# Performance work log

Hardware: AMD Instinct MI355X
Metric: run time of the kernel (lower is better)

Reference implementation:

```python
import jax, jax.numpy as jnp
import numpy as np

H = 128        # hidden_size
L = 3          # n_layers
VOCAB = 256    # input_size == output_size


def setup_inputs() -> dict:
    key = jax.random.key(0)
    ks = jax.random.split(key, 10)
    s = 1.0 / np.sqrt(H)  # PyTorch LSTM/Linear init scale
    return {
        "x": jax.random.randint(ks[0], (1,), 0, VOCAB),
        "h0": jax.random.normal(ks[1], (L, 1, H), dtype=jnp.float32),
        "c0": jax.random.normal(ks[2], (L, 1, H), dtype=jnp.float32),
        # params
        "emb": jax.random.normal(ks[3], (VOCAB, H), dtype=jnp.float32),
        "w_ih": jax.random.uniform(ks[4], (L, 4 * H, H), minval=-s, maxval=s, dtype=jnp.float32),
        "w_hh": jax.random.uniform(ks[5], (L, 4 * H, H), minval=-s, maxval=s, dtype=jnp.float32),
        "b_ih": jax.random.uniform(ks[6], (L, 4 * H), minval=-s, maxval=s, dtype=jnp.float32),
        "b_hh": jax.random.uniform(ks[7], (L, 4 * H), minval=-s, maxval=s, dtype=jnp.float32),
        "Wd": jax.random.uniform(ks[8], (VOCAB, H), minval=-s, maxval=s, dtype=jnp.float32),
        "bd": jax.random.uniform(ks[9], (VOCAB,), minval=-s, maxval=s, dtype=jnp.float32),
    }


def _lstm_step(inp, h0, c0, w_ih, w_hh, b_ih, b_hh):
    """Single time-step, 3-layer LSTM. inp: [1,H]; h0,c0: [L,1,H]. Dropout in eval mode (identity)."""
    hs, cs = [], []
    h_in = inp
    for l in range(L):
        # PyTorch gate order: input, forget, cell(g), output
        gates = h_in @ w_ih[l].T + h0[l] @ w_hh[l].T + b_ih[l] + b_hh[l]  # [1, 4H]
        i, f, g, o = jnp.split(gates, 4, axis=-1)
        c = jax.nn.sigmoid(f) * c0[l] + jax.nn.sigmoid(i) * jnp.tanh(g)
        h = jax.nn.sigmoid(o) * jnp.tanh(c)
        hs.append(h)
        cs.append(c)
        h_in = h  # inter-layer dropout (p=0.5) is identity in eval mode
    return h_in, jnp.stack(hs), jnp.stack(cs)


def reference(x, h0, c0, emb, w_ih, w_hh, b_ih, b_hh, Wd, bd):
    inp = emb[x].reshape(1, H)                      # encoder: [1, H]
    out, hn, cn = _lstm_step(inp, h0, c0, w_ih, w_hh, b_ih, b_hh)
    # self.dropout(p=0.1) identity in eval mode
    logits = out @ Wd.T + bd                        # decoder: [1, VOCAB]
    return logits, hn, cn
```

## Files before the change

### kernel.cpp

```cpp
#include <hip/hip_runtime.h>
#include <math.h>

#define H 128
#define NL 3
#define VOCAB 256
#define NBL 8
#define NLB (NL*NBL)
#define ND 2
#define NB_TOT (NLB+ND)

#define K_TAG(l) (0x51C0DE00u + (unsigned)(l))

typedef unsigned long long u64;

__device__ __forceinline__ float sigmoidf_(float x) {
    return 1.0f / (1.0f + __expf(-x));
}
__device__ __forceinline__ float fast_tanhf(float x) {
    const float e = __expf(2.0f * x);
    return 1.0f - 2.0f * __frcp_rn(e + 1.0f);
}

__global__ __launch_bounds__(256) void fused_lstm_kernel(
    const int*   __restrict__ x_idx,
    const float* __restrict__ h0,
    const float* __restrict__ c0,
    const float* __restrict__ emb,
    const float* __restrict__ w_ih,
    const float* __restrict__ w_hh,
    const float* __restrict__ b_ih,
    const float* __restrict__ b_hh,
    const float* __restrict__ Wd,
    const float* __restrict__ bd,
    float* __restrict__ logits,
    float* __restrict__ hn,
    float* __restrict__ cn,
    u64*   __restrict__ slots)
{
    __shared__ float s_in[H];
    __shared__ float s_h[H];

    const int t   = threadIdx.x;
    const int bid = blockIdx.x;

    if (bid < NLB) {
        const int l  = bid >> 3;
        const int gb = bid & 7;

        const int ul    = t >> 4;
        const int g     = (t >> 2) & 3;
        const int chunk = t & 3;
        const int unit  = gb * 16 + ul;
        const int grow  = g * H + unit;

        const size_t base = ((size_t)l * 4 * H + grow) * H + chunk * 32;
        const float4* pi = (const float4*)(w_ih + base);
        const float4* ph = (const float4*)(w_hh + base);
        float4 wih[8], whh[8];
#pragma unroll
        for (int i = 0; i < 8; ++i) { wih[i] = pi[i]; whh[i] = ph[i]; }
        float bias = 0.0f;
        if (chunk == 0) bias = b_ih[(size_t)l * 4 * H + grow]
                             + b_hh[(size_t)l * 4 * H + grow];
        float c0reg = 0.0f;
        if ((t & 15) == 0) c0reg = c0[l * H + unit];

        if (t >= 128) {
            const int tl = t - 128;
            s_h[tl] = h0[l * H + tl];
            if (l == 0) s_in[tl] = emb[(size_t)x_idx[0] * H + tl];
        }
        __syncthreads();

        const float4* sh = (const float4*)s_h + chunk * 8;
        float r = bias;
#pragma unroll
        for (int i = 0; i < 8; ++i) {
            float4 a = whh[i], v = sh[i];
            r = fmaf(a.x, v.x, r);  r = fmaf(a.y, v.y, r);
            r = fmaf(a.z, v.z, r);  r = fmaf(a.w, v.w, r);
        }

        if (l > 0) {
            if (t < H) {
                const unsigned want = K_TAG(l - 1);
                u64 v;
                do {
                    v = __hip_atomic_load(&slots[(l - 1) * H + t],
                                          __ATOMIC_RELAXED,
                                          __HIP_MEMORY_SCOPE_AGENT);
                } while ((unsigned)(v >> 32) != want);
                s_in[t] = __uint_as_float((unsigned)v);
            }
        }
        __syncthreads();

        const float4* si = (const float4*)s_in + chunk * 8;
        float acc = r;
#pragma unroll
        for (int i = 0; i < 8; ++i) {
            float4 a = wih[i], v = si[i];
            acc = fmaf(a.x, v.x, acc);  acc = fmaf(a.y, v.y, acc);
            acc = fmaf(a.z, v.z, acc);  acc = fmaf(a.w, v.w, acc);
        }
        acc += __shfl_xor(acc, 1);
        acc += __shfl_xor(acc, 2);
        const int bl = (t & 63) & 48;
        const float iv = __shfl(acc, bl,      64);
        const float fv = __shfl(acc, bl + 4,  64);
        const float gv = __shfl(acc, bl + 8,  64);
        const float ov = __shfl(acc, bl + 12, 64);
        if ((t & 15) == 0) {
            const float c = sigmoidf_(fv) * c0reg + sigmoidf_(iv) * fast_tanhf(gv);
            const float h = sigmoidf_(ov) * fast_tanhf(c);
            cn[l * H + unit] = c;
            hn[l * H + unit] = h;
            const u64 w = ((u64)K_TAG(l) << 32) | (u64)__float_as_uint(h);
            __hip_atomic_store(&slots[l * H + unit], w,
                               __ATOMIC_RELAXED, __HIP_MEMORY_SCOPE_AGENT);
        }
    } else {
        const int db        = bid - NLB;
        const int row_local = t >> 1;
        const int chunk     = t & 1;
        const int drow      = db * 128 + row_local;

        const float4* pw = (const float4*)(Wd + (size_t)drow * H + chunk * 64);
        float4 wd[16];
#pragma unroll
        for (int i = 0; i < 16; ++i) wd[i] = pw[i];
        const float bias = bd[drow];
        asm volatile("" ::: "memory");

        if (t < H) {
            const unsigned want = K_TAG(2);
            u64 v;
            do {
                v = __hip_atomic_load(&slots[2 * H + t],
                                      __ATOMIC_RELAXED,
                                      __HIP_MEMORY_SCOPE_AGENT);
            } while ((unsigned)(v >> 32) != want);
            s_in[t] = __uint_as_float((unsigned)v);
        }
        __syncthreads();

        const float4* sh = (const float4*)s_in + chunk * 16;
        float acc = 0.0f;
#pragma unroll
        for (int i = 0; i < 16; ++i) {
            float4 a = wd[i], v = sh[i];
            acc = fmaf(a.x, v.x, acc); acc = fmaf(a.y, v.y, acc);
            acc = fmaf(a.z, v.z, acc); acc = fmaf(a.w, v.w, acc);
        }
        acc += __shfl_xor(acc, 1);
        if (chunk == 0) logits[drow] = acc + bias;
    }
}

extern "C" void kernel_launch(void* const* d_in, const int* in_sizes, int n_in,
                              void* d_out, int out_size, void* d_ws, size_t ws_size,
                              hipStream_t stream) {
    const int*   x    = (const int*)  d_in[0];
    const float* h0   = (const float*)d_in[1];
    const float* c0   = (const float*)d_in[2];
    const float* emb  = (const float*)d_in[3];
    const float* w_ih = (const float*)d_in[4];
    const float* w_hh = (const float*)d_in[5];
    const float* b_ih = (const float*)d_in[6];
    const float* b_hh = (const float*)d_in[7];
    const float* Wd   = (const float*)d_in[8];
    const float* bd   = (const float*)d_in[9];

    float* out    = (float*)d_out;
    float* logits = out;
    float* hn     = out + VOCAB;
    float* cn     = hn + NL * H;

    u64* slots = (u64*)d_ws;

    fused_lstm_kernel<<<NB_TOT, 256, 0, stream>>>(
        x, h0, c0, emb, w_ih, w_hh, b_ih, b_hh, Wd, bd,
        logits, hn, cn, slots);
}
```

Before: 10.82 us.

## Double LSTM blocks per layer, load h0 into registers, gather gates via shared memory

Splits each layer across 16 blocks of 8 hidden units instead of 8 blocks of 16, halving the per-thread weight slice to 16 elements per matrix and spreading the weight loads over more CUs. h0 is read straight into registers, which removes the shared-memory staging and the first block barrier. Gate values are now collected through a small shared array plus an extra barrier instead of cross-lane shuffles. This trades more blocks spinning on the inter-layer flags, and one added barrier, for lower per-block load latency.

```diff
diff --git a/kernel.cpp b/kernel.cpp
--- a/kernel.cpp
+++ b/kernel.cpp
@@ -4,7 +4,7 @@
 #define H 128
 #define NL 3
 #define VOCAB 256
-#define NBL 8
+#define NBL 16
 #define NLB (NL*NBL)
 #define ND 2
 #define NB_TOT (NLB+ND)
@@ -38,45 +38,40 @@
     u64*   __restrict__ slots)
 {
     __shared__ float s_in[H];
-    __shared__ float s_h[H];
+    __shared__ float s_gates[4][8];
 
     const int t   = threadIdx.x;
     const int bid = blockIdx.x;
 
     if (bid < NLB) {
-        const int l  = bid >> 3;
-        const int gb = bid & 7;
+        const int l  = bid >> 4;
+        const int gb = bid & 15;
 
-        const int ul    = t >> 4;
-        const int g     = (t >> 2) & 3;
-        const int chunk = t & 3;
-        const int unit  = gb * 16 + ul;
-        const int grow  = g * H + unit;
+        const int row_local = t >> 3;
+        const int chunk     = t & 7;
+        const int g    = row_local >> 3;
+        const int jr   = row_local & 7;
+        const int unit = gb * 8 + jr;
+        const int grow = g * H + unit;
 
-        const size_t base = ((size_t)l * 4 * H + grow) * H + chunk * 32;
+        const size_t base = ((size_t)l * 4 * H + grow) * H + chunk * 16;
         const float4* pi = (const float4*)(w_ih + base);
         const float4* ph = (const float4*)(w_hh + base);
-        float4 wih[8], whh[8];
+        const float4* p0 = (const float4*)(h0 + l * H + chunk * 16);
+        float4 wih[4], whh[4], h0v[4];
 #pragma unroll
-        for (int i = 0; i < 8; ++i) { wih[i] = pi[i]; whh[i] = ph[i]; }
+        for (int i = 0; i < 4; ++i) { wih[i] = pi[i]; whh[i] = ph[i]; h0v[i] = p0[i]; }
         float bias = 0.0f;
         if (chunk == 0) bias = b_ih[(size_t)l * 4 * H + grow]
                              + b_hh[(size_t)l * 4 * H + grow];
         float c0reg = 0.0f;
-        if ((t & 15) == 0) c0reg = c0[l * H + unit];
+        if (t < 8) c0reg = c0[l * H + gb * 8 + t];
+        if (l == 0 && t < H) s_in[t] = emb[(size_t)x_idx[0] * H + t];
 
-        if (t >= 128) {
-            const int tl = t - 128;
-            s_h[tl] = h0[l * H + tl];
-            if (l == 0) s_in[tl] = emb[(size_t)x_idx[0] * H + tl];
-        }
-        __syncthreads();
-
-        const float4* sh = (const float4*)s_h + chunk * 8;
         float r = bias;
 #pragma unroll
-        for (int i = 0; i < 8; ++i) {
-            float4 a = whh[i], v = sh[i];
+        for (int i = 0; i < 4; ++i) {
+            float4 a = whh[i], v = h0v[i];
             r = fmaf(a.x, v.x, r);  r = fmaf(a.y, v.y, r);
             r = fmaf(a.z, v.z, r);  r = fmaf(a.w, v.w, r);
         }
@@ -95,28 +90,32 @@
         }
         __syncthreads();
 
-        const float4* si = (const float4*)s_in + chunk * 8;
+        const float4* si = (const float4*)s_in + chunk * 4;
         float acc = r;
 #pragma unroll
-        for (int i = 0; i < 8; ++i) {
+        for (int i = 0; i < 4; ++i) {
             float4 a = wih[i], v = si[i];
             acc = fmaf(a.x, v.x, acc);  acc = fmaf(a.y, v.y, acc);
             acc = fmaf(a.z, v.z, acc);  acc = fmaf(a.w, v.w, acc);
         }
         acc += __shfl_xor(acc, 1);
         acc += __shfl_xor(acc, 2);
-        const int bl = (t & 63) & 48;
-        const float iv = __shfl(acc, bl,      64);
-        const float fv = __shfl(acc, bl + 4,  64);
-        const float gv = __shfl(acc, bl + 8,  64);
-        const float ov = __shfl(acc, bl + 12, 64);
-        if ((t & 15) == 0) {
+        acc += __shfl_xor(acc, 4);
+        if (chunk == 0) s_gates[g][jr] = acc;
+        __syncthreads();
+
+        if (t < 8) {
+            const int u = gb * 8 + t;
+            const float iv = s_gates[0][t];
+            const float fv = s_gates[1][t];
+            const float gv = s_gates[2][t];
+            const float ov = s_gates[3][t];
             const float c = sigmoidf_(fv) * c0reg + sigmoidf_(iv) * fast_tanhf(gv);
             const float h = sigmoidf_(ov) * fast_tanhf(c);
-            cn[l * H + unit] = c;
-            hn[l * H + unit] = h;
+            cn[l * H + u] = c;
+            hn[l * H + u] = h;
             const u64 w = ((u64)K_TAG(l) << 32) | (u64)__float_as_uint(h);
-            __hip_atomic_store(&slots[l * H + unit], w,
+            __hip_atomic_store(&slots[l * H + u], w,
                                __ATOMIC_RELAXED, __HIP_MEMORY_SCOPE_AGENT);
         }
     } else {
```

Measured after the change: 12.33 us. 13.9% more time.
